# Kernel tuning notes

Hardware: AMD Instinct MI355X
Metric: run time of the kernel (lower is better)

## Reference

```python
import jax, jax.numpy as jnp
import numpy as np

WIN = (4, 16)
HEADS = 4
DIM = 128
HID = 512

def _rel_index(win):
    ch = np.arange(win[0]); cw = np.arange(win[1])
    coords = np.stack(np.meshgrid(ch, cw, indexing='ij')).reshape(2, -1)  # 2, N
    rel = (coords[:, :, None] - coords[:, None, :]).transpose(1, 2, 0).astype(np.int64)  # N,N,2
    rel[:, :, 0] += win[0] - 1
    rel[:, :, 1] += win[1] - 1
    rel[:, :, 0] *= 2 * win[1] - 1
    return jnp.asarray(rel.sum(-1))  # (N, N) int

REL_IDX = _rel_index(WIN)

def _ln(x, g, b):
    m = x.mean(-1, keepdims=True)
    v = ((x - m) ** 2).mean(-1, keepdims=True)
    return (x - m) / jnp.sqrt(v + 1e-5) * g + b

def _gelu(x):
    return jax.nn.gelu(x, approximate=False)

def _posconv3d(x, w, b):
    # depthwise 3x3x3 conv with singleton depth axis; x: B,C,H,W; w: C,1,3,3,3
    y = jax.lax.conv_general_dilated(x[:, :, None], w, (1, 1, 1), ((1, 1), (1, 1), (1, 1)),
                                     feature_group_count=x.shape[1],
                                     dimension_numbers=('NCDHW', 'OIDHW', 'NCDHW'))
    return y[:, :, 0] + b[None, :, None, None]

def _dwconv2d(x, w, b):
    # depthwise 3x3 conv; x: B,Ch,H,W; w: Ch,1,3,3
    y = jax.lax.conv_general_dilated(x, w, (1, 1), ((1, 1), (1, 1)),
                                     feature_group_count=x.shape[1],
                                     dimension_numbers=('NCHW', 'OIHW', 'NCHW'))
    return y + b[None, :, None, None]

def setup_inputs() -> dict:
    key = jax.random.key(0)
    ks = jax.random.split(key, 12)
    B, C, H, W = 4, DIM, 192, 192
    s = 0.02
    return {
        'x': jax.random.normal(ks[0], (B, C, H, W), jnp.float32),
        'pos_w': jax.random.normal(ks[1], (C, 1, 3, 3, 3), jnp.float32) * s,
        'pos_b': jnp.zeros((C,), jnp.float32),
        'ln1_g': jnp.ones((C,), jnp.float32),
        'ln1_b': jnp.zeros((C,), jnp.float32),
        'q_w': jax.random.normal(ks[2], (C, C), jnp.float32) * s,
        'q_b': jnp.zeros((C,), jnp.float32),
        'kv_w': jax.random.normal(ks[3], (C, 2 * C), jnp.float32) * s,
        'kv_b': jnp.zeros((2 * C,), jnp.float32),
        'rpb': jax.random.normal(ks[4], ((2 * WIN[0] - 1) * (2 * WIN[1] - 1), HEADS), jnp.float32) * s,
        'proj_w': jax.random.normal(ks[5], (C, C), jnp.float32) * s,
        'proj_b': jnp.zeros((C,), jnp.float32),
        'fft1_w': jax.random.normal(ks[6], (2 * C, 2 * C), jnp.float32) * s,
        'fft1_b': jnp.zeros((2 * C,), jnp.float32),
        'fft2_w': jax.random.normal(ks[7], (2 * C, 2 * C), jnp.float32) * s,
        'fft2_b': jnp.zeros((2 * C,), jnp.float32),
        'ln2_g': jnp.ones((C,), jnp.float32),
        'ln2_b': jnp.zeros((C,), jnp.float32),
        'l1_w': jax.random.normal(ks[8], (C, HID), jnp.float32) * s,
        'l1_b': jnp.zeros((HID,), jnp.float32),
        'dw_w': jax.random.normal(ks[9], (HID, 1, 3, 3), jnp.float32) * s,
        'dw_b': jnp.zeros((HID,), jnp.float32),
        'l2_w': jax.random.normal(ks[10], (HID, C), jnp.float32) * s,
        'l2_b': jnp.zeros((C,), jnp.float32),
    }

def _forward(x, pos_w, pos_b, ln1_g, ln1_b, q_w, q_b, kv_w, kv_b, rpb, proj_w, proj_b,
             fft1_w, fft1_b, fft2_w, fft2_b, ln2_g, ln2_b, l1_w, l1_b, dw_w, dw_b, l2_w, l2_b):
    B, C, H, W = x.shape
    wh, ww = WIN
    N = wh * ww
    hd = C // HEADS
    # depthwise 3D positional embedding
    x = x + _posconv3d(x, pos_w, pos_b)
    xt = x.transpose(0, 2, 3, 1)  # B,H,W,C
    shortcut = xt
    xn = _ln(xt, ln1_g, ln1_b)
    # window partition: (B*nW, N, C)  (idx=0 -> no shift, no mask)
    win = xn.reshape(B, H // wh, wh, W // ww, ww, C).transpose(0, 1, 3, 2, 4, 5).reshape(-1, N, C)
    q = (win @ q_w + q_b).reshape(-1, N, HEADS, hd).transpose(0, 2, 1, 3)  # Bw,h,N,d
    kv = (win @ kv_w + kv_b).reshape(-1, N, 2, HEADS, hd).transpose(2, 0, 3, 1, 4)
    k, v = kv[0], kv[1]
    attn = jnp.einsum('bhnd,bhmd->bhnm', q * (hd ** -0.5), k)
    rel_bias = rpb[REL_IDX].transpose(2, 0, 1)  # heads,N,N
    attn = jax.nn.softmax(attn + rel_bias[None], axis=-1)
    out = jnp.einsum('bhnm,bhmd->bhnd', attn, v).transpose(0, 2, 1, 3).reshape(-1, N, C)
    out = out @ proj_w + proj_b
    out = out.reshape(B, H // wh, W // ww, wh, ww, C).transpose(0, 1, 3, 2, 4, 5).reshape(B, H, W, C)
    xt = shortcut + out
    # FFT residual branch (two 1x1 convs on cat(real,imag))
    xc = xt.transpose(0, 3, 1, 2)  # B,C,H,W
    f = jnp.fft.rfft2(xc, axes=(-2, -1))
    ff = jnp.concatenate([f.real, f.imag], axis=1)  # B,2C,H,Wf
    ff = jnp.einsum('bchw,co->bohw', ff, fft1_w) + fft1_b[None, :, None, None]
    ff = jnp.where(ff >= 0, ff, 0.01 * ff)  # LeakyReLU(0.01)
    ff = jnp.einsum('bchw,co->bohw', ff, fft2_w) + fft2_b[None, :, None, None]
    fr, fi = jnp.split(ff, 2, axis=1)
    y = jnp.fft.irfft2(fr + 1j * fi, s=(H, W), axes=(-2, -1))
    xt = xt + y.transpose(0, 2, 3, 1)
    # LeFF: linear -> dwconv -> linear, on full (H,W) grid
    xn2 = _ln(xt, ln2_g, ln2_b)
    h1 = _gelu(xn2 @ l1_w + l1_b)               # B,H,W,HID
    h1 = _gelu(_dwconv2d(h1.transpose(0, 3, 1, 2), dw_w, dw_b))
    h2 = h1.transpose(0, 2, 3, 1) @ l2_w + l2_b  # B,H,W,C
    xt = xt + h2
    return xt.transpose(0, 3, 1, 2)

def reference(x, pos_w, pos_b, ln1_g, ln1_b, q_w, q_b, kv_w, kv_b, rpb, proj_w, proj_b,
              fft1_w, fft1_b, fft2_w, fft2_b, ln2_g, ln2_b, l1_w, l1_b, dw_w, dw_b, l2_w, l2_b):
    return _forward(x, pos_w, pos_b, ln1_g, ln1_b, q_w, q_b, kv_w, kv_b, rpb, proj_w, proj_b,
                    fft1_w, fft1_b, fft2_w, fft2_b, ln2_g, ln2_b, l1_w, l1_b, dw_w, dw_b, l2_w, l2_b)
```

## Files before the change

### kernel.cpp

```cpp
#include <hip/hip_runtime.h>
#include <hip/hip_bf16.h>
#include <math.h>

#define C_DIM 128
#define HGT 192
#define WID 192
#define NB 4
#define WFD 97

#define T_BIAS  0
#define T_QKVB  16384
#define TF_SZ   16896
#define UT_MW    0
#define UT_MHF   49152
#define UT_MHI   196608
#define UT_MWI   344064
#define UT_QKVW  387072
#define UT_PROJW 436224
#define UT_FFT1W 452608
#define UT_FFT2W 518144
#define UT_L1W   583680
#define UT_L2W   649216
#define UT_TOT   714752
#define TAB_SZ   374272

typedef __attribute__((ext_vector_type(8))) short bf16x8;
typedef __attribute__((ext_vector_type(4))) float f32x4;

__device__ __forceinline__ float gelu_f(float v){
  return 0.5f*v*(1.0f + erff(v*0.70710678118654752440f));
}
__device__ __forceinline__ unsigned short f2bf(float f){
  __hip_bfloat16 h = __float2bfloat16(f);
  return *reinterpret_cast<unsigned short*>(&h);
}
__device__ __forceinline__ float bf2f(unsigned short u){
  unsigned int x = ((unsigned int)u)<<16;
  return __uint_as_float(x);
}
__device__ __forceinline__ void st8u(unsigned short* d, bf16x8 v){
  unsigned int* wp = (unsigned int*)&v;
  unsigned int* dp = (unsigned int*)d;
  dp[0]=wp[0]; dp[1]=wp[1]; dp[2]=wp[2]; dp[3]=wp[3];
}

__global__ __launch_bounds__(256) void build_tables(float* __restrict__ tab,
        const float* __restrict__ rpb, const float* __restrict__ q_b, const float* __restrict__ kv_b,
        const float* __restrict__ q_w, const float* __restrict__ kv_w, const float* __restrict__ proj_w,
        const float* __restrict__ fft1_w, const float* __restrict__ fft2_w,
        const float* __restrict__ l1_w, const float* __restrict__ l2_w){
  int idx = blockIdx.x*256 + threadIdx.x;
  const float STEP = (float)(6.283185307179586476925286766559/192.0);
  if (idx < 16384){
    int head = idx>>12, n = (idx>>6)&63, m = idx&63;
    int dh = n/16 - m/16 + 3;
    int dw = (n&15) - (m&15) + 15;
    tab[T_BIAS+idx] = rpb[(dh*31+dw)*4 + head];
    return;
  }
  idx -= 16384;
  if (idx < 384){
    tab[T_QKVB+idx] = (idx < 128) ? q_b[idx] : kv_b[idx-128];
    return;
  }
  idx -= 384;
  unsigned short* ut = (unsigned short*)(tab + TF_SZ);
  if (idx < 49152){
    int r = idx/192, w = idx%192;
    float v = 0.f;
    if (r < 97){ int a = (r*w)%192; v = cosf(a*STEP); }
    else if (r < 194){ int a = ((r-97)*w)%192; v = -sinf(a*STEP); }
    ut[UT_MW+idx] = f2bf(v);
    return;
  }
  idx -= 49152;
  if (idx < 147456){
    int r = idx/384, j = idx%384;
    int hf = (r < 192) ? r : r-192;
    int h  = (j < 192) ? j : j-192;
    int a = (hf*h)%192;
    float c = cosf(a*STEP), s = sinf(a*STEP);
    float v;
    if (r < 192) v = (j < 192) ? c : s;
    else         v = (j < 192) ? -s : c;
    ut[UT_MHF+idx] = f2bf(v);
    return;
  }
  idx -= 147456;
  if (idx < 147456){
    int r = idx/384, j = idx%384;
    int h  = (r < 192) ? r : r-192;
    int hf = (j < 192) ? j : j-192;
    int a = (h*hf)%192;
    float c = cosf(a*STEP), s = sinf(a*STEP);
    float v;
    if (r < 192) v = (j < 192) ? c : -s;
    else         v = (j < 192) ? s : c;
    ut[UT_MHI+idx] = f2bf(v);
    return;
  }
  idx -= 147456;
  if (idx < 43008){
    int w = idx/224, j = idx%224;
    float v = 0.f;
    if (j < 97){
      int a = (j*w)%192;
      float sc = ((j==0 || j==96) ? 1.f : 2.f) / 36864.f;
      v = sc*cosf(a*STEP);
    } else if (j >= 112 && j < 209){
      int k = j-112;
      int a = (k*w)%192;
      float sc = ((k==0 || k==96) ? 1.f : 2.f) / 36864.f;
      v = -sc*sinf(a*STEP);
    }
    ut[UT_MWI+idx] = f2bf(v);
    return;
  }
  idx -= 43008;
  if (idx < 49152){
    int n = idx/128, k = idx%128;
    float v = (n < 128) ? q_w[(size_t)k*128 + n] : kv_w[(size_t)k*256 + (n-128)];
    ut[UT_QKVW+idx] = f2bf(v);
    return;
  }
  idx -= 49152;
  if (idx < 16384){
    int n = idx/128, k = idx%128;
    ut[UT_PROJW+idx] = f2bf(proj_w[(size_t)k*128 + n]);
    return;
  }
  idx -= 16384;
  if (idx < 65536){
    int n = idx/256, k = idx%256;
    ut[UT_FFT1W+idx] = f2bf(fft1_w[(size_t)k*256 + n]);
    return;
  }
  idx -= 65536;
  if (idx < 65536){
    int n = idx/256, k = idx%256;
    ut[UT_FFT2W+idx] = f2bf(fft2_w[(size_t)k*256 + n]);
    return;
  }
  idx -= 65536;
  if (idx < 65536){
    int n = idx/128, k = idx%128;
    ut[UT_L1W+idx] = f2bf(l1_w[(size_t)k*512 + n]);
    return;
  }
  idx -= 65536;
  if (idx < 65536){
    int n = idx/512, k = idx%512;
    ut[UT_L2W+idx] = f2bf(l2_w[(size_t)k*128 + n]);
  }
}

__global__ __launch_bounds__(256) void posconv3_kernel(const float* __restrict__ x, const float* __restrict__ pw,
                               const float* __restrict__ pb, float* __restrict__ xt){
  __shared__ float rows_s[16*340];
  int w0 = blockIdx.x*32, h0 = blockIdx.y*8;
  int b = blockIdx.z >> 3, cb = (blockIdx.z & 7)*16;
  int tid = threadIdx.x;
  int hl = tid >> 5, wl = tid & 31;
  for (int e = tid; e < 16*340; e += 256){
    int c = e / 340; int rem = e - c*340;
    int r = rem / 34; int wc = rem - r*34;
    int gh = h0 - 1 + r, gw = w0 - 1 + wc;
    float v = 0.f;
    if (gh >= 0 && gh < HGT && gw >= 0 && gw < WID)
      v = x[((size_t)(b*C_DIM + cb + c))*(HGT*WID) + gh*WID + gw];
    rows_s[e] = v;
  }
  __syncthreads();
  float outr[16];
  #pragma unroll
  for (int c = 0; c < 16; ++c){
    const float* rs = &rows_s[c*340];
    float wreg[9];
    #pragma unroll
    for (int t9 = 0; t9 < 9; ++t9) wreg[t9] = pw[(cb+c)*27 + 9 + t9];
    float bias = pb[cb+c];
    float acc = rs[(hl+1)*34 + wl+1] + bias;
    #pragma unroll
    for (int ky = 0; ky < 3; ++ky)
      #pragma unroll
      for (int kx = 0; kx < 3; ++kx)
        acc += wreg[ky*3+kx]*rs[(hl+ky)*34 + wl+kx];
    outr[c] = acc;
  }
  __syncthreads();
  {
    int px = hl*32 + wl;
    #pragma unroll
    for (int c = 0; c < 16; ++c) rows_s[px*17 + c] = outr[c];
  }
  __syncthreads();
  for (int r = 0; r < 16; ++r){
    int e = r*256 + tid;
    int cl = e & 15, hw = e >> 4;
    int h = hw >> 5, w = hw & 31;
    xt[((size_t)(b*HGT + h0+h)*WID + (w0+w))*C_DIM + cb + cl] = rows_s[hw*17 + cl];
  }
}

__global__ __launch_bounds__(256) void ln_stats_kernel(const float* __restrict__ src, float* __restrict__ stats){
  int wave = threadIdx.x >> 6; int lane = threadIdx.x & 63;
  size_t p = (size_t)blockIdx.x*4 + wave;
  const float* s = src + p*C_DIM;
  float v0 = s[lane], v1 = s[lane+64];
  float sum = v0 + v1;
  #pragma unroll
  for (int o=1; o<64; o<<=1) sum += __shfl_xor(sum, o, 64);
  float m = sum * (1.0f/128.0f);
  float d0 = v0-m, d1 = v1-m;
  float vs = d0*d0 + d1*d1;
  #pragma unroll
  for (int o=1; o<64; o<<=1) vs += __shfl_xor(vs, o, 64);
  float rstd = rsqrtf(vs*(1.0f/128.0f) + 1e-5f);
  if (lane==0){ stats[2*p] = m; stats[2*p+1] = rstd; }
}

template<int ACT, bool ADD, bool LNA, bool ABF, bool OBF, int NT, bool OUTT = false>
__global__ __launch_bounds__(256) void gemm2(const void* __restrict__ A1v,
                            const unsigned short* __restrict__ WT, const float* __restrict__ bias,
                            void* __restrict__ dstv, int K, int N, int lda,
                            const float* __restrict__ stats, const float* __restrict__ lng,
                            const float* __restrict__ lnb, int prow0, int pmax){
  __shared__ __align__(16) unsigned short As[64*40];
  __shared__ __align__(16) unsigned short Bs[NT][64*40];
  __shared__ float tileT[OUTT ? 64*66 : 1];
  int p0 = blockIdx.y*64, n00 = blockIdx.x*(64*NT);
  int tid = threadIdx.x;
  int wave = tid >> 6, lane = tid & 63;
  int wr = (wave>>1)*32, wc = (wave&1)*32;
  f32x4 acc[NT][4];
  #pragma unroll
  for (int nt=0; nt<NT; ++nt)
    #pragma unroll
    for (int q=0; q<4; ++q) acc[nt][q] = (f32x4){};
  int am = tid >> 2, ak = (tid & 3)*8;
  int brow = tid >> 2, bkk = (tid & 3)*8;
  for (int k0 = 0; k0 < K; k0 += 32){
    if constexpr (ABF){
      const unsigned short* A1u = (const unsigned short*)A1v;
      bf16x8 av = *(const bf16x8*)(A1u + (size_t)(p0+am)*lda + k0 + ak);
      st8u(&As[am*40 + ak], av);
    } else {
      int gp = p0 + am;
      float s0 = 0.f, s1 = 0.f;
      if (LNA){
        gp += prow0;
        gp = gp < 0 ? 0 : (gp > pmax ? pmax : gp);
        s0 = stats[2*gp]; s1 = stats[2*gp+1];
      }
      const float* src = (const float*)A1v + (size_t)gp*lda + k0 + ak;
      float4 aa = *(const float4*)src;
      float4 ab = *(const float4*)(src+4);
      float v[8] = {aa.x,aa.y,aa.z,aa.w,ab.x,ab.y,ab.z,ab.w};
      unsigned short* dp = &As[am*40 + ak];
      #pragma unroll
      for (int j=0;j<8;j++){
        float f = v[j];
        if (LNA) f = (f - s0)*s1*lng[k0+ak+j] + lnb[k0+ak+j];
        dp[j] = f2bf(f);
      }
    }
    #pragma unroll
    for (int nt=0; nt<NT; ++nt){
      bf16x8 wv = *(const bf16x8*)(WT + (size_t)(n00 + nt*64 + brow)*K + k0 + bkk);
      st8u(&Bs[nt][brow*40 + bkk], wv);
    }
    __syncthreads();
    int fm = lane & 15, kg = (lane>>4)*8;
    bf16x8 a0 = *(const bf16x8*)&As[(wr+fm)*40 + kg];
    bf16x8 a1 = *(const bf16x8*)&As[(wr+16+fm)*40 + kg];
    #pragma unroll
    for (int nt=0; nt<NT; ++nt){
      bf16x8 b0 = *(const bf16x8*)&Bs[nt][(wc+fm)*40 + kg];
      bf16x8 b1 = *(const bf16x8*)&Bs[nt][(wc+16+fm)*40 + kg];
      acc[nt][0] = __builtin_amdgcn_mfma_f32_16x16x32_bf16(a0, b0, acc[nt][0], 0,0,0);
      acc[nt][1] = __builtin_amdgcn_mfma_f32_16x16x32_bf16(a0, b1, acc[nt][1], 0,0,0);
      acc[nt][2] = __builtin_amdgcn_mfma_f32_16x16x32_bf16(a1, b0, acc[nt][2], 0,0,0);
      acc[nt][3] = __builtin_amdgcn_mfma_f32_16x16x32_bf16(a1, b1, acc[nt][3], 0,0,0);
    }
    __syncthreads();
  }
  int cn = lane & 15, rq = (lane>>4)*4;
  if constexpr (OUTT){
    const float* XTres = stats;
    int p0b = prow0 + p0;
    #pragma unroll
    for (int mi=0; mi<2; ++mi){
      #pragma unroll
      for (int ni=0; ni<2; ++ni){
        f32x4 a = acc[0][mi*2+ni];
        int nl = wc + ni*16 + cn;
        float bsv = bias[n00 + nl];
        #pragma unroll
        for (int r=0; r<4; ++r){
          int rowl = wr + mi*16 + rq + r;
          float v = a[r] + bsv;
          v += XTres[(size_t)(p0b + rowl)*C_DIM + n00 + nl];
          tileT[rowl*66 + nl] = v;
        }
      }
    }
    __syncthreads();
    int bb = p0b/36864;
    int hh = (p0b/192)%192;
    int w0 = p0b%192;
    float* dout = (float*)dstv;
    #pragma unroll
    for (int it=0; it<16; ++it){
      int e = it*256 + tid;
      int c = e >> 6, wl = e & 63;
      dout[((size_t)bb*C_DIM + n00 + c)*36864 + (size_t)hh*192 + w0 + wl] = tileT[wl*66 + c];
    }
  } else {
    #pragma unroll
    for (int nt=0; nt<NT; ++nt){
      #pragma unroll
      for (int mi=0; mi<2; ++mi){
        #pragma unroll
        for (int ni=0; ni<2; ++ni){
          f32x4 a = acc[nt][mi*2+ni];
          int n = n00 + nt*64 + wc + ni*16 + cn;
          float bsv = bias[n];
          #pragma unroll
          for (int r=0; r<4; ++r){
            size_t row = (size_t)p0 + wr + mi*16 + rq + r;
            float v = a[r] + bsv;
            if (ACT==1) v = (v>=0.f) ? v : 0.01f*v;
            if (ACT==2) v = gelu_f(v);
            if constexpr (OBF){
              ((unsigned short*)dstv)[row*(size_t)N + n] = f2bf(v);
            } else {
              float* dst = (float*)dstv;
              if (ADD) v += dst[row*(size_t)N + n];
              dst[row*(size_t)N + n] = v;
            }
          }
        }
      }
    }
  }
}

template<int MODE>
__global__ __launch_bounds__(256) void dft_gemm(const unsigned short* __restrict__ Atab,
                            const void* __restrict__ W1v, const void* __restrict__ W2v,
                            void* __restrict__ D1v, void* __restrict__ D2v, int k0){
  constexpr int K      = (MODE==0)?192 : (MODE==3)?224 : 384;
  constexpr int MT     = (MODE==0)?4 : (MODE==3)?3 : 6;
  constexpr int MVALID = (MODE==0)?194 : (MODE==3)?192 : 384;
  __shared__ __align__(16) unsigned short As[64*40];
  __shared__ __align__(16) unsigned short Bs[64*40];
  int slab = blockIdx.y / MT;
  int p0 = (blockIdx.y % MT)*64, n0 = blockIdx.x*64;
  int tid = threadIdx.x;
  int wave = tid >> 6, lane = tid & 63;
  int wr = (wave>>1)*32, wc = (wave&1)*32;
  f32x4 acc00 = {}, acc01 = {}, acc10 = {}, acc11 = {};
  int am = tid >> 2, ak = (tid & 3)*8;
  int bk = tid >> 3, bn = (tid & 7)*8;
  for (int kk0 = 0; kk0 < K; kk0 += 32){
    {
      bf16x8 av = *(const bf16x8*)(Atab + (size_t)(p0+am)*K + kk0 + ak);
      st8u(&As[am*40 + ak], av);
    }
    {
      int r = kk0 + bk;
      if (MODE==0){
        const float* src = (const float*)W1v + (size_t)slab*24576 + (size_t)r*128 + n0 + bn;
        float4 wa = *(const float4*)src;
        float4 wb = *(const float4*)(src+4);
        float v[8] = {wa.x,wa.y,wa.z,wa.w,wb.x,wb.y,wb.z,wb.w};
        #pragma unroll
        for (int j=0;j<8;j++) Bs[(bn+j)*40 + bk] = f2bf(v[j]);
      } else {
        const unsigned short* src;
        if (MODE==1) src = (r<192) ? (const unsigned short*)W1v + (size_t)(k0+slab)*128 + (size_t)r*12416
                                   : (const unsigned short*)W2v + (size_t)(k0+slab)*128 + (size_t)(r-192)*12416;
        else if (MODE==2) src = (r<192) ? (const unsigned short*)W1v + (size_t)slab*49152 + (size_t)r*256
                                        : (const unsigned short*)W2v + (size_t)slab*49152 + (size_t)(r-192)*256;
        else src = (r<112) ? (const unsigned short*)W1v + (size_t)slab*24832 + (size_t)r*256
                           : (const unsigned short*)W2v + (size_t)slab*24832 + (size_t)(r-112)*256;
        src += n0 + bn;
        bf16x8 wv = *(const bf16x8*)src;
        #pragma unroll
        for (int j=0;j<8;j++) Bs[(bn+j)*40 + bk] = (unsigned short)wv[j];
      }
    }
    __syncthreads();
    int fm = lane & 15, kg = (lane>>4)*8;
    bf16x8 a0 = *(const bf16x8*)&As[(wr+fm)*40 + kg];
    bf16x8 a1 = *(const bf16x8*)&As[(wr+16+fm)*40 + kg];
    bf16x8 b0 = *(const bf16x8*)&Bs[(wc+fm)*40 + kg];
    bf16x8 b1 = *(const bf16x8*)&Bs[(wc+16+fm)*40 + kg];
    acc00 = __builtin_amdgcn_mfma_f32_16x16x32_bf16(a0, b0, acc00, 0,0,0);
    acc01 = __builtin_amdgcn_mfma_f32_16x16x32_bf16(a0, b1, acc01, 0,0,0);
    acc10 = __builtin_amdgcn_mfma_f32_16x16x32_bf16(a1, b0, acc10, 0,0,0);
    acc11 = __builtin_amdgcn_mfma_f32_16x16x32_bf16(a1, b1, acc11, 0,0,0);
    __syncthreads();
  }
  int cn = lane & 15, rq = (lane>>4)*4;
  #pragma unroll
  for (int mi=0; mi<2; ++mi){
    #pragma unroll
    for (int ni=0; ni<2; ++ni){
      f32x4 a = (mi==0) ? (ni==0?acc00:acc01) : (ni==0?acc10:acc11);
      int n = n0 + wc + ni*16 + cn;
      #pragma unroll
      for (int r=0; r<4; ++r){
        int p = p0 + wr + mi*16 + rq + r;
        if (p >= MVALID) continue;
        float v = a[r];
        if (MODE==0){
          unsigned short* D1 = (unsigned short*)D1v;
          unsigned short* D2 = (unsigned short*)D2v;
          if (p < 97) D1[(size_t)slab*12416 + (size_t)p*128 + n] = f2bf(v);
          else        D2[(size_t)slab*12416 + (size_t)(p-97)*128 + n] = f2bf(v);
        } else if (MODE==1){
          unsigned short* base = (unsigned short*)D1v + (size_t)slab*49152;
          if (p < 192) base[(size_t)p*256 + n] = f2bf(v);
          else         base[(size_t)(p-192)*256 + 128 + n] = f2bf(v);
        } else if (MODE==2){
          unsigned short* D1 = (unsigned short*)D1v;
          int kg2 = k0 + slab;
          if (p < 192) D1[((size_t)p*97 + kg2)*256 + n] = f2bf(v);
          else         D1[((size_t)(p-192)*97 + kg2)*256 + 128 + n] = f2bf(v);
        } else {
          ((float*)D1v)[(size_t)slab*24576 + (size_t)p*128 + n] += v;
        }
      }
    }
  }
}

#define XS_OFF  0
#define WQK_OFF 8704
#define VT_OFF  29184
#define SHM_TOT 38400
__global__ __launch_bounds__(256) void attn_fused3(
    float* __restrict__ XT, const float* __restrict__ stats,
    const float* __restrict__ g1, const float* __restrict__ b1,
    const unsigned short* __restrict__ QKVW, const float* __restrict__ QKVB,
    const float* __restrict__ biasT, const unsigned short* __restrict__ PROJW,
    const float* __restrict__ projb){
  __shared__ __align__(16) unsigned short shm[SHM_TOT];
  int win = blockIdx.x;
  int b = win/576, rem = win%576, whi = rem/12, wwi = rem%12;
  int tid = threadIdx.x, wave = tid>>6, lane = tid&63, head = wave;
  int fm = lane & 15, kg = (lane>>4)*8;
  size_t rowbase = (size_t)(b*HGT + whi*4)*WID + wwi*16;
  {
    int t = tid >> 2;
    int c0 = (tid & 3)*32;
    size_t grow = rowbase + (size_t)(t>>4)*WID + (t&15);
    const float* src = XT + grow*C_DIM + c0;
    float m = stats[2*grow], rs = stats[2*grow+1];
    unsigned short* dst = &shm[XS_OFF + t*136 + c0];
    #pragma unroll
    for (int j=0;j<32;j++){
      float f = (src[j]-m)*rs*g1[c0+j] + b1[c0+j];
      dst[j] = f2bf(f);
    }
  }
  __syncthreads();
  unsigned short* Qw = &shm[WQK_OFF + wave*5120];
  unsigned short* Kw = Qw + 2560;
  unsigned short* Vt = &shm[VT_OFF + wave*2304];
  #pragma unroll
  for (int op=0; op<3; ++op){
    f32x4 acc[4][2];
    #pragma unroll
    for (int tf=0; tf<4; ++tf){ acc[tf][0] = (f32x4){}; acc[tf][1] = (f32x4){}; }
    int wrow0 = op*128 + head*32;
    #pragma unroll
    for (int kk0=0; kk0<128; kk0+=32){
      bf16x8 bfr0 = *(const bf16x8*)(QKVW + (size_t)(wrow0 + fm)*128 + kk0 + kg);
      bf16x8 bfr1 = *(const bf16x8*)(QKVW + (size_t)(wrow0 + 16 + fm)*128 + kk0 + kg);
      #pragma unroll
      for (int tf=0; tf<4; ++tf){
        bf16x8 af = *(const bf16x8*)&shm[XS_OFF + (tf*16+fm)*136 + kk0 + kg];
        acc[tf][0] = __builtin_amdgcn_mfma_f32_16x16x32_bf16(af, bfr0, acc[tf][0], 0,0,0);
        acc[tf][1] = __builtin_amdgcn_mfma_f32_16x16x32_bf16(af, bfr1, acc[tf][1], 0,0,0);
      }
    }
    #pragma unroll
    for (int tf=0; tf<4; ++tf){
      #pragma unroll
      for (int cf=0; cf<2; ++cf){
        int n = cf*16 + fm;
        float bsv = QKVB[op*128 + head*32 + n];
        #pragma unroll
        for (int r=0;r<4;r++){
          int token = tf*16 + (lane>>4)*4 + r;
          float v = acc[tf][cf][r] + bsv;
          if (op==0) v *= 0.17677669529663688f;
          unsigned short bv = f2bf(v);
          if (op==0)      Qw[token*40 + n] = bv;
          else if (op==1) Kw[token*40 + n] = bv;
          else            Vt[n*72 + token] = bv;
        }
      }
    }
  }
  __syncthreads();
  bf16x8 qf[4], kf[4];
  #pragma unroll
  for (int t4=0; t4<4; ++t4){
    qf[t4] = *(const bf16x8*)&Qw[(t4*16+fm)*40 + kg];
    kf[t4] = *(const bf16x8*)&Kw[(t4*16+fm)*40 + kg];
  }
  f32x4 s[4][4];
  #pragma unroll
  for (int ni=0; ni<4; ++ni)
    #pragma unroll
    for (int mj=0; mj<4; ++mj){
      f32x4 z = {};
      s[ni][mj] = __builtin_amdgcn_mfma_f32_16x16x32_bf16(qf[ni], kf[mj], z, 0,0,0);
    }
  const float* bp = biasT + head*4096;
  #pragma unroll
  for (int ni=0; ni<4; ++ni){
    int nbase = ni*16 + (lane>>4)*4;
    #pragma unroll
    for (int mj=0; mj<4; ++mj){
      int m = mj*16 + fm;
      #pragma unroll
      for (int r=0;r<4;r++)
        s[ni][mj][r] += bp[(nbase+r)*64 + m];
    }
  }
  float rs_[4][4];
  #pragma unroll
  for (int ni=0; ni<4; ++ni){
    #pragma unroll
    for (int r=0;r<4;r++){
      float t = fmaxf(fmaxf(s[ni][0][r], s[ni][1][r]), fmaxf(s[ni][2][r], s[ni][3][r]));
      #pragma unroll
      for (int o=1;o<16;o<<=1) t = fmaxf(t, __shfl_xor(t, o, 64));
      float sum = 0.f;
      #pragma unroll
      for (int mj=0; mj<4; ++mj){
        float e = __expf(s[ni][mj][r] - t);
        s[ni][mj][r] = e;
        sum += e;
      }
      #pragma unroll
      for (int o=1;o<16;o<<=1) sum += __shfl_xor(sum, o, 64);
      rs_[ni][r] = sum;
    }
  }
  __syncthreads();
  unsigned short* Ps = Qw;
  #pragma unroll
  for (int ni=0; ni<4; ++ni){
    int nbase = ni*16 + (lane>>4)*4;
    #pragma unroll
    for (int mj=0; mj<4; ++mj){
      int m = mj*16 + fm;
      #pragma unroll
      for (int r=0;r<4;r++)
        Ps[(nbase+r)*72 + m] = f2bf(s[ni][mj][r]);
    }
  }
  f32x4 o2[4][2];
  #pragma unroll
  for (int ni=0; ni<4; ++ni){ o2[ni][0] = (f32x4){}; o2[ni][1] = (f32x4){}; }
  #pragma unroll
  for (int ks=0; ks<2; ++ks){
    bf16x8 vb0 = *(const bf16x8*)&Vt[fm*72 + ks*32+kg];
    bf16x8 vb1 = *(const bf16x8*)&Vt[(16+fm)*72 + ks*32+kg];
    #pragma unroll
    for (int ni=0; ni<4; ++ni){
      bf16x8 pa = *(const bf16x8*)&Ps[(ni*16+fm)*72 + ks*32+kg];
      o2[ni][0] = __builtin_amdgcn_mfma_f32_16x16x32_bf16(pa, vb0, o2[ni][0], 0,0,0);
      o2[ni][1] = __builtin_amdgcn_mfma_f32_16x16x32_bf16(pa, vb1, o2[ni][1], 0,0,0);
    }
  }
  #pragma unroll
  for (int ni=0; ni<4; ++ni){
    #pragma unroll
    for (int r=0;r<4;r++){
      int token = ni*16 + (lane>>4)*4 + r;
      float inv = 1.0f / rs_[ni][r];
      unsigned short* op = &shm[XS_OFF + token*136 + head*32];
      op[fm]    = f2bf(o2[ni][0][r]*inv);
      op[16+fm] = f2bf(o2[ni][1][r]*inv);
    }
  }
  __syncthreads();
  {
    f32x4 pacc[4][2];
    #pragma unroll
    for (int tf=0; tf<4; ++tf){ pacc[tf][0] = (f32x4){}; pacc[tf][1] = (f32x4){}; }
    int wrow0 = wave*32;
    #pragma unroll
    for (int kk0=0; kk0<128; kk0+=32){
      bf16x8 bfr0 = *(const bf16x8*)(PROJW + (size_t)(wrow0 + fm)*128 + kk0 + kg);
      bf16x8 bfr1 = *(const bf16x8*)(PROJW + (size_t)(wrow0 + 16 + fm)*128 + kk0 + kg);
      #pragma unroll
      for (int tf=0; tf<4; ++tf){
        bf16x8 af = *(const bf16x8*)&shm[XS_OFF + (tf*16+fm)*136 + kk0 + kg];
        pacc[tf][0] = __builtin_amdgcn_mfma_f32_16x16x32_bf16(af, bfr0, pacc[tf][0], 0,0,0);
        pacc[tf][1] = __builtin_amdgcn_mfma_f32_16x16x32_bf16(af, bfr1, pacc[tf][1], 0,0,0);
      }
    }
    #pragma unroll
    for (int tf=0; tf<4; ++tf){
      #pragma unroll
      for (int cf=0; cf<2; ++cf){
        int n = wave*32 + cf*16 + fm;
        float bsv = projb[n];
        #pragma unroll
        for (int r=0;r<4;r++){
          size_t l = rowbase + (size_t)tf*WID + (lane>>4)*4 + r;
          XT[l*C_DIM + n] += pacc[tf][cf][r] + bsv;
        }
      }
    }
  }
}

__global__ __launch_bounds__(256) void dwconv_strip(const unsigned short* __restrict__ SB1,
                                                    const float* __restrict__ dw,
                                                    const float* __restrict__ db,
                                                    unsigned short* __restrict__ SB2,
                                                    int r0){
  int blk = blockIdx.x;
  int wt = blk % 12, hl = blk / 12;
  int tid = threadIdx.x;
  int c4 = tid & 127, ph = tid >> 7;
  int ch = c4*4;
  int w0 = wt*16 + ph*8;
  int h = r0 + hl;
  float wreg[9][4], bias[4];
  #pragma unroll
  for (int j=0;j<4;j++){
    bias[j] = db[ch+j];
    #pragma unroll
    for (int t9=0;t9<9;t9++) wreg[t9][j] = dw[(ch+j)*9+t9];
  }
  const unsigned short* rp[3];
  bool rv[3];
  #pragma unroll
  for (int ky=0;ky<3;ky++){
    int hh = h + ky - 1;
    rv[ky] = (hh >= 0) && (hh < HGT);
    rp[ky] = SB1 + ((size_t)(hl+ky)*WID)*512 + ch;
  }
  float win[3][3][4];
  #pragma unroll
  for (int ky=0;ky<3;ky++){
    #pragma unroll
    for (int j=0;j<4;j++){ win[ky][0][j]=0.f; win[ky][1][j]=0.f; }
    if (rv[ky]){
      if (w0 > 0){
        const unsigned int* p = (const unsigned int*)(rp[ky] + (size_t)(w0-1)*512);
        unsigned int u0=p[0], u1=p[1];
        win[ky][0][0]=bf2f((unsigned short)(u0&0xFFFF)); win[ky][0][1]=bf2f((unsigned short)(u0>>16));
        win[ky][0][2]=bf2f((unsigned short)(u1&0xFFFF)); win[ky][0][3]=bf2f((unsigned short)(u1>>16));
      }
      {
        const unsigned int* p = (const unsigned int*)(rp[ky] + (size_t)w0*512);
        unsigned int u0=p[0], u1=p[1];
        win[ky][1][0]=bf2f((unsigned short)(u0&0xFFFF)); win[ky][1][1]=bf2f((unsigned short)(u0>>16));
        win[ky][1][2]=bf2f((unsigned short)(u1&0xFFFF)); win[ky][1][3]=bf2f((unsigned short)(u1>>16));
      }
    }
  }
  #pragma unroll
  for (int px=0; px<8; ++px){
    int w = w0 + px;
    #pragma unroll
    for (int ky=0;ky<3;ky++){
      #pragma unroll
      for (int j=0;j<4;j++) win[ky][2][j]=0.f;
      if (rv[ky] && (w+1) < WID){
        const unsigned int* p = (const unsigned int*)(rp[ky] + (size_t)(w+1)*512);
        unsigned int u0=p[0], u1=p[1];
        win[ky][2][0]=bf2f((unsigned short)(u0&0xFFFF)); win[ky][2][1]=bf2f((unsigned short)(u0>>16));
        win[ky][2][2]=bf2f((unsigned short)(u1&0xFFFF)); win[ky][2][3]=bf2f((unsigned short)(u1>>16));
      }
    }
    float a[4];
    #pragma unroll
    for (int j=0;j<4;j++){
      float acc = bias[j];
      #pragma unroll
      for (int ky=0;ky<3;ky++)
        #pragma unroll
        for (int kx=0;kx<3;kx++)
          acc += wreg[ky*3+kx][j]*win[ky][kx][j];
      a[j] = gelu_f(acc);
    }
    unsigned int o0 = (unsigned int)f2bf(a[0]) | ((unsigned int)f2bf(a[1])<<16);
    unsigned int o1 = (unsigned int)f2bf(a[2]) | ((unsigned int)f2bf(a[3])<<16);
    unsigned int* op = (unsigned int*)&SB2[((size_t)hl*WID + w)*512 + ch];
    op[0] = o0; op[1] = o1;
    #pragma unroll
    for (int ky=0;ky<3;ky++)
      #pragma unroll
      for (int j=0;j<4;j++){ win[ky][0][j]=win[ky][1][j]; win[ky][1][j]=win[ky][2][j]; }
  }
}

__global__ __launch_bounds__(256) void transpose_b_kernel(const float* __restrict__ src, float* __restrict__ dst,
                                                          size_t zstride){
  __shared__ float tile[128*65];
  int w0 = blockIdx.x*64, h = blockIdx.y;
  size_t zo = (size_t)blockIdx.z * zstride;
  int tid = threadIdx.x;
  for (int r=0; r<32; r++){
    int e = tid + 256*r; int c = e & 127, wl = e >> 7;
    tile[c*65 + wl] = src[zo + ((size_t)h*WID + w0 + wl)*C_DIM + c];
  }
  __syncthreads();
  for (int r=0; r<32; r++){
    int e = tid + 256*r; int wl = e & 63, c = e >> 6;
    dst[zo + ((size_t)c*HGT + h)*WID + w0 + wl] = tile[c*65 + wl];
  }
}

extern "C" void kernel_launch(void* const* d_in, const int* in_sizes, int n_in,
                              void* d_out, int out_size, void* d_ws, size_t ws_size,
                              hipStream_t stream) {
  const float* x      = (const float*)d_in[0];
  const float* pos_w  = (const float*)d_in[1];
  const float* pos_b  = (const float*)d_in[2];
  const float* ln1_g  = (const float*)d_in[3];
  const float* ln1_b  = (const float*)d_in[4];
  const float* q_w    = (const float*)d_in[5];
  const float* q_b    = (const float*)d_in[6];
  const float* kv_w   = (const float*)d_in[7];
  const float* kv_b   = (const float*)d_in[8];
  const float* rpb    = (const float*)d_in[9];
  const float* proj_w = (const float*)d_in[10];
  const float* proj_b = (const float*)d_in[11];
  const float* fft1_w = (const float*)d_in[12];
  const float* fft1_b = (const float*)d_in[13];
  const float* fft2_w = (const float*)d_in[14];
  const float* fft2_b = (const float*)d_in[15];
  const float* ln2_g  = (const float*)d_in[16];
  const float* ln2_b  = (const float*)d_in[17];
  const float* l1_w   = (const float*)d_in[18];
  const float* l1_b   = (const float*)d_in[19];
  const float* dw_w   = (const float*)d_in[20];
  const float* dw_b   = (const float*)d_in[21];
  const float* l2_w   = (const float*)d_in[22];
  const float* l2_b   = (const float*)d_in[23];

  const size_t S   = (size_t)NB*HGT*WID*C_DIM;
  const size_t Sb  = S/NB;
  const size_t SZb = (size_t)HGT*WFD*C_DIM;
  const size_t GSZ = (size_t)HGT*WFD*256;
  const int    P   = (int)(NB*HGT*WID);

  float* ws    = (float*)d_ws;
  float* TAB   = ws;
  float* STATS = ws + TAB_SZ;
  float* POOL  = ws + TAB_SZ + 2*(size_t)P;
  size_t head  = TAB_SZ + 2*(size_t)P;
  size_t pool  = (ws_size/4 > head) ? (ws_size/4 - head) : 0;

  bool xt_in_pool = (pool >= S + 5200000);
  float* XT     = xt_in_pool ? POOL : (float*)d_out;
  float* POOL2  = xt_in_pool ? POOL + S : POOL;
  size_t pool2  = xt_in_pool ? pool - S : pool;

  const float* biasT = TAB + T_BIAS;
  const float* QKVB  = TAB + T_QKVB;
  const unsigned short* UT = (const unsigned short*)(TAB + TF_SZ);
  const unsigned short* MW  = UT + UT_MW;
  const unsigned short* MHF = UT + UT_MHF;
  const unsigned short* MHI = UT + UT_MHI;
  const unsigned short* MWI = UT + UT_MWI;
  const unsigned short* QKVW  = UT + UT_QKVW;
  const unsigned short* PROJW = UT + UT_PROJW;
  const unsigned short* FFT1W = UT + UT_FFT1W;
  const unsigned short* FFT2W = UT + UT_FFT2W;
  const unsigned short* L1W   = UT + UT_L1W;
  const unsigned short* L2W   = UT + UT_L2W;

  build_tables<<<2858, 256, 0, stream>>>(TAB, rpb, q_b, kv_b, q_w, kv_w, proj_w,
                                         fft1_w, fft2_w, l1_w, l2_w);
  posconv3_kernel<<<dim3(6,24,32), 256, 0, stream>>>(x, pos_w, pos_b, XT);

  ln_stats_kernel<<<P/4, 256, 0, stream>>>(XT, STATS);
  attn_fused3<<<2304, 256, 0, stream>>>(XT, STATS, ln1_g, ln1_b, QKVW, QKVB,
                                        biasT, PROJW, proj_b);

  {
    unsigned short* FRu = (unsigned short*)POOL2;
    unsigned short* FIu = FRu + SZb;
    unsigned short* Gu  = FIu + SZb;
    size_t fixed = SZb + GSZ/2;
    int CK;
    unsigned short* FF0u;
    unsigned short* FF1u;
    if (xt_in_pool){
      CK = WFD;
      FF0u = (unsigned short*)d_out;
      FF1u = FF0u + (size_t)WFD*49152;
    } else {
      int CKmax = 1;
      if (pool2 > fixed + 49152) CKmax = (int)((pool2 - fixed)/49152);
      if (CKmax < 1) CKmax = 1;
      if (CKmax > WFD) CKmax = WFD;
      int nch = (WFD + CKmax - 1)/CKmax;
      CK = (WFD + nch - 1)/nch;
      FF0u = (unsigned short*)(POOL2 + fixed);
      FF1u = FF0u + (size_t)CK*49152;
    }
    for (int b = 0; b < NB; ++b){
      float* XTb = XT + (size_t)b*Sb;
      dft_gemm<0><<<dim3(2, 192*4), 256, 0, stream>>>(MW, XTb, nullptr, FRu, FIu, 0);
      for (int k0 = 0; k0 < WFD; k0 += CK){
        int ck = (WFD - k0 < CK) ? (WFD - k0) : CK;
        int rows = ck*192;
        dft_gemm<1><<<dim3(2, ck*6), 256, 0, stream>>>(MHF, FRu, FIu, FF0u, nullptr, k0);
        gemm2<1,false,false,true,true,1><<<dim3(4, rows/64), 256, 0, stream>>>(
            FF0u, FFT1W, fft1_b, FF1u, 256, 256, 256, nullptr, nullptr, nullptr, 0, 0);
        gemm2<0,false,false,true,true,1><<<dim3(4, rows/64), 256, 0, stream>>>(
            FF1u, FFT2W, fft2_b, FF0u, 256, 256, 256, nullptr, nullptr, nullptr, 0, 0);
        dft_gemm<2><<<dim3(2, ck*6), 256, 0, stream>>>(MHI, FF0u, FF0u+128, Gu, nullptr, k0);
      }
      dft_gemm<3><<<dim3(2, 192*3), 256, 0, stream>>>(MWI, Gu, Gu+128, XTb, nullptr, 0);
    }
  }

  ln_stats_kernel<<<P/4, 256, 0, stream>>>(XT, STATS);

  {
    int SH = 96;
    while ((size_t)(3*SH+4)*49152 > pool2 && SH > 24) SH >>= 1;
    const size_t SB1SZ = (size_t)(SH+2)*98304;
    unsigned short* SB1u[2] = { (unsigned short*)POOL2, (unsigned short*)POOL2 + SB1SZ };
    unsigned short* SB2u = (unsigned short*)POOL2 + 2*SB1SZ;
    int nStrips = HGT/SH;
    for (int b = 0; b < NB; ++b){
      auto launch_g = [&](int s){
        int r0 = s*SH;
        int prow0 = (b*HGT + r0 - 1)*WID;
        gemm2<2,false,true,false,true,2><<<dim3(4, (SH+2)*3), 256, 0, stream>>>(
            XT, L1W, l1_b, SB1u[s&1], 128, 512, 128,
            STATS, ln2_g, ln2_b, prow0, P-1);
      };
      launch_g(0);
      for (int s = 0; s < nStrips; ++s){
        if (s+1 < nStrips) launch_g(s+1);
        int r0 = s*SH;
        dwconv_strip<<<12*SH, 256, 0, stream>>>(SB1u[s&1], dw_w, dw_b, SB2u, r0);
        if (xt_in_pool){
          gemm2<0,false,false,true,false,1,true><<<dim3(2, SH*3), 256, 0, stream>>>(
              SB2u, L2W, l2_b, d_out, 512, 128, 512,
              XT, nullptr, nullptr, (b*HGT + r0)*WID, 0);
        } else {
          gemm2<0,true,false,true,false,1><<<dim3(2, SH*3), 256, 0, stream>>>(
              SB2u, L2W, l2_b, XT + ((size_t)(b*HGT + r0)*WID)*C_DIM,
              512, 128, 512, nullptr, nullptr, nullptr, 0, 0);
        }
      }
    }
  }

  if (!xt_in_pool){
    for (int b = 0; b < NB; ++b){
      transpose_b_kernel<<<dim3(3,192,1), 256, 0, stream>>>(XT + (size_t)b*Sb, POOL2, 0);
      hipMemcpyAsync((float*)d_out + (size_t)b*Sb, POOL2, Sb*sizeof(float),
                     hipMemcpyDeviceToDevice, stream);
    }
  }
}
```

Baseline: 1.112 ms.

## Load GEMM operand fragments directly from global memory, dropping LDS staging

In gemm2, the A and B tiles are no longer staged through shared memory. Each wave loads its MFMA fragments straight from global memory and applies the LayerNorm/bf16 conversion in registers, so both __syncthreads calls go away. In dft_gemm, the A table is likewise read directly from global memory while B still goes through LDS. This removes LDS traffic and barriers but loses data sharing across waves, so each element is fetched from global/L2 several times. The A reads in the float path are also recomputed redundantly, including repeated LayerNorm work per wave.

```diff
diff --git a/kernel.cpp b/kernel.cpp
--- a/kernel.cpp
+++ b/kernel.cpp
@@ -225,64 +225,68 @@
                             void* __restrict__ dstv, int K, int N, int lda,
                             const float* __restrict__ stats, const float* __restrict__ lng,
                             const float* __restrict__ lnb, int prow0, int pmax){
-  __shared__ __align__(16) unsigned short As[64*40];
-  __shared__ __align__(16) unsigned short Bs[NT][64*40];
   __shared__ float tileT[OUTT ? 64*66 : 1];
   int p0 = blockIdx.y*64, n00 = blockIdx.x*(64*NT);
   int tid = threadIdx.x;
   int wave = tid >> 6, lane = tid & 63;
   int wr = (wave>>1)*32, wc = (wave&1)*32;
+  int fm = lane & 15, kg = (lane>>4)*8;
   f32x4 acc[NT][4];
   #pragma unroll
   for (int nt=0; nt<NT; ++nt)
     #pragma unroll
     for (int q=0; q<4; ++q) acc[nt][q] = (f32x4){};
-  int am = tid >> 2, ak = (tid & 3)*8;
-  int brow = tid >> 2, bkk = (tid & 3)*8;
+  const float* A1f = (const float*)A1v;
+  const unsigned short* A1u = (const unsigned short*)A1v;
+  int gA0 = p0 + wr + fm;
+  int gA1 = gA0 + 16;
+  float s0a = 0.f, s1a = 0.f, s0b = 0.f, s1b = 0.f;
+  if constexpr (LNA){
+    gA0 += prow0; gA0 = gA0 < 0 ? 0 : (gA0 > pmax ? pmax : gA0);
+    gA1 += prow0; gA1 = gA1 < 0 ? 0 : (gA1 > pmax ? pmax : gA1);
+    s0a = stats[2*gA0]; s1a = stats[2*gA0+1];
+    s0b = stats[2*gA1]; s1b = stats[2*gA1+1];
+  }
   for (int k0 = 0; k0 < K; k0 += 32){
+    bf16x8 a0, a1;
     if constexpr (ABF){
-      const unsigned short* A1u = (const unsigned short*)A1v;
-      bf16x8 av = *(const bf16x8*)(A1u + (size_t)(p0+am)*lda + k0 + ak);
-      st8u(&As[am*40 + ak], av);
+      a0 = *(const bf16x8*)(A1u + (size_t)gA0*lda + k0 + kg);
+      a1 = *(const bf16x8*)(A1u + (size_t)gA1*lda + k0 + kg);
     } else {
-      int gp = p0 + am;
-      float s0 = 0.f, s1 = 0.f;
-      if (LNA){
-        gp += prow0;
-        gp = gp < 0 ? 0 : (gp > pmax ? pmax : gp);
-        s0 = stats[2*gp]; s1 = stats[2*gp+1];
-      }
-      const float* src = (const float*)A1v + (size_t)gp*lda + k0 + ak;
-      float4 aa = *(const float4*)src;
-      float4 ab = *(const float4*)(src+4);
-      float v[8] = {aa.x,aa.y,aa.z,aa.w,ab.x,ab.y,ab.z,ab.w};
-      unsigned short* dp = &As[am*40 + ak];
-      #pragma unroll
-      for (int j=0;j<8;j++){
-        float f = v[j];
-        if (LNA) f = (f - s0)*s1*lng[k0+ak+j] + lnb[k0+ak+j];
-        dp[j] = f2bf(f);
+      {
+        const float* src = A1f + (size_t)gA0*lda + k0 + kg;
+        float4 aa = *(const float4*)src;
+        float4 ab = *(const float4*)(src+4);
+        float v[8] = {aa.x,aa.y,aa.z,aa.w,ab.x,ab.y,ab.z,ab.w};
+        #pragma unroll
+        for (int j=0;j<8;j++){
+          float f = v[j];
+          if (LNA) f = (f - s0a)*s1a*lng[k0+kg+j] + lnb[k0+kg+j];
+          a0[j] = (short)f2bf(f);
+        }
+      }
+      {
+        const float* src = A1f + (size_t)gA1*lda + k0 + kg;
+        float4 aa = *(const float4*)src;
+        float4 ab = *(const float4*)(src+4);
+        float v[8] = {aa.x,aa.y,aa.z,aa.w,ab.x,ab.y,ab.z,ab.w};
+        #pragma unroll
+        for (int j=0;j<8;j++){
+          float f = v[j];
+          if (LNA) f = (f - s0b)*s1b*lng[k0+kg+j] + lnb[k0+kg+j];
+          a1[j] = (short)f2bf(f);
+        }
       }
     }
     #pragma unroll
     for (int nt=0; nt<NT; ++nt){
-      bf16x8 wv = *(const bf16x8*)(WT + (size_t)(n00 + nt*64 + brow)*K + k0 + bkk);
-      st8u(&Bs[nt][brow*40 + bkk], wv);
-    }
-    __syncthreads();
-    int fm = lane & 15, kg = (lane>>4)*8;
-    bf16x8 a0 = *(const bf16x8*)&As[(wr+fm)*40 + kg];
-    bf16x8 a1 = *(const bf16x8*)&As[(wr+16+fm)*40 + kg];
-    #pragma unroll
-    for (int nt=0; nt<NT; ++nt){
-      bf16x8 b0 = *(const bf16x8*)&Bs[nt][(wc+fm)*40 + kg];
-      bf16x8 b1 = *(const bf16x8*)&Bs[nt][(wc+16+fm)*40 + kg];
+      bf16x8 b0 = *(const bf16x8*)(WT + (size_t)(n00 + nt*64 + wc + fm)*K + k0 + kg);
+      bf16x8 b1 = *(const bf16x8*)(WT + (size_t)(n00 + nt*64 + wc + 16 + fm)*K + k0 + kg);
       acc[nt][0] = __builtin_amdgcn_mfma_f32_16x16x32_bf16(a0, b0, acc[nt][0], 0,0,0);
       acc[nt][1] = __builtin_amdgcn_mfma_f32_16x16x32_bf16(a0, b1, acc[nt][1], 0,0,0);
       acc[nt][2] = __builtin_amdgcn_mfma_f32_16x16x32_bf16(a1, b0, acc[nt][2], 0,0,0);
       acc[nt][3] = __builtin_amdgcn_mfma_f32_16x16x32_bf16(a1, b1, acc[nt][3], 0,0,0);
     }
-    __syncthreads();
   }
   int cn = lane & 15, rq = (lane>>4)*4;
   if constexpr (OUTT){
@@ -352,21 +356,16 @@
   constexpr int K      = (MODE==0)?192 : (MODE==3)?224 : 384;
   constexpr int MT     = (MODE==0)?4 : (MODE==3)?3 : 6;
   constexpr int MVALID = (MODE==0)?194 : (MODE==3)?192 : 384;
-  __shared__ __align__(16) unsigned short As[64*40];
   __shared__ __align__(16) unsigned short Bs[64*40];
   int slab = blockIdx.y / MT;
   int p0 = (blockIdx.y % MT)*64, n0 = blockIdx.x*64;
   int tid = threadIdx.x;
   int wave = tid >> 6, lane = tid & 63;
   int wr = (wave>>1)*32, wc = (wave&1)*32;
+  int fm = lane & 15, kg = (lane>>4)*8;
   f32x4 acc00 = {}, acc01 = {}, acc10 = {}, acc11 = {};
-  int am = tid >> 2, ak = (tid & 3)*8;
   int bk = tid >> 3, bn = (tid & 7)*8;
   for (int kk0 = 0; kk0 < K; kk0 += 32){
-    {
-      bf16x8 av = *(const bf16x8*)(Atab + (size_t)(p0+am)*K + kk0 + ak);
-      st8u(&As[am*40 + ak], av);
-    }
     {
       int r = kk0 + bk;
       if (MODE==0){
@@ -391,9 +390,8 @@
       }
     }
     __syncthreads();
-    int fm = lane & 15, kg = (lane>>4)*8;
-    bf16x8 a0 = *(const bf16x8*)&As[(wr+fm)*40 + kg];
-    bf16x8 a1 = *(const bf16x8*)&As[(wr+16+fm)*40 + kg];
+    bf16x8 a0 = *(const bf16x8*)(Atab + (size_t)(p0+wr+fm)*K + kk0 + kg);
+    bf16x8 a1 = *(const bf16x8*)(Atab + (size_t)(p0+wr+16+fm)*K + kk0 + kg);
     bf16x8 b0 = *(const bf16x8*)&Bs[(wc+fm)*40 + kg];
     bf16x8 b1 = *(const bf16x8*)&Bs[(wc+16+fm)*40 + kg];
     acc00 = __builtin_amdgcn_mfma_f32_16x16x32_bf16(a0, b0, acc00, 0,0,0);
```

After: 1.377 ms. 1.24x slower.
